# Optimization experiments

Hardware: AMD Instinct MI355X
Metric: run time of the kernel (lower is better)

The kernel has to match this reference:

```python
import jax, jax.numpy as jnp
import numpy as np

# GE2E batch structure: N_SPK speakers, M_UTT utterances each (grouped contiguously),
# first half enrollment (-> centroid), second half test.
N_SPK, M_UTT, D = 1024, 32, 512
M_ENR = M_UTT // 2
EPS = 1e-8  # F.cosine_similarity default eps (clamps norms)


def setup_inputs() -> dict:
    key = jax.random.key(0)
    emb = jax.random.normal(key, (N_SPK * M_UTT, D), dtype=jnp.float32)
    labels = jnp.repeat(jnp.arange(N_SPK, dtype=jnp.int64), M_UTT)
    alpha = jnp.asarray(10.0, dtype=jnp.float32)
    beta = jnp.asarray(-5.0, dtype=jnp.float32)
    return {"embeddings": emb, "labels": labels, "alpha": alpha, "beta": beta}


def reference(embeddings, labels, alpha, beta):
    # labels are contiguously grouped: label i occupies rows [i*M_UTT, (i+1)*M_UTT)
    emb = embeddings.reshape(N_SPK, M_UTT, D)
    enroll = emb[:, :M_ENR]          # [N, M_enr, D]
    test = emb[:, M_ENR:]            # [N, M_tst, D]
    centroid = enroll.mean(axis=1)   # [N, D]

    cent_n = centroid / jnp.maximum(
        jnp.linalg.norm(centroid, axis=-1, keepdims=True), EPS)
    test_n = test / jnp.maximum(
        jnp.linalg.norm(test, axis=-1, keepdims=True), EPS)

    # S[i, j, t] = alpha * cos(centroid_i, test_{j,t}) + beta
    S = alpha * jnp.einsum('id,jtd->ijt', cent_n, test_n) + beta
    E = jnp.exp(S)                                   # [N, N, M_tst]

    idx = jnp.arange(N_SPK)
    pos_sum = E[idx, idx].sum(axis=-1)               # diag: own test vs own centroid
    neg_sum = E.sum(axis=(1, 2)) - pos_sum           # all other speakers' test utts

    loss = (jnp.log(neg_sum) - jnp.log(pos_sum)).mean()
    return loss
```

## Files before the change

kernel.cpp:

```cpp
#include <hip/hip_runtime.h>
#include <math.h>

#define N_SPK 1024
#define M_UTT 32
#define M_ENR 16
#define M_TEST 16
#define D 512
#define N_TEST_ROWS (N_SPK * M_TEST)


typedef __attribute__((ext_vector_type(4))) float f32x4;
typedef __attribute__((ext_vector_type(8))) short short8;
typedef __attribute__((ext_vector_type(8))) unsigned short ushort8;

typedef const __attribute__((address_space(1))) void g_void;
typedef __attribute__((address_space(3))) void lds_void;

__device__ __forceinline__ unsigned short f2bf(float f) {
    unsigned int u = __float_as_uint(f);
    u += 0x7FFF + ((u >> 16) & 1);
    return (unsigned short)(u >> 16);
}

__global__ __launch_bounds__(256) void prep_kernel(const float* __restrict__ emb,
                                                   unsigned short* __restrict__ cent,
                                                   unsigned short* __restrict__ test,
                                                   float* __restrict__ g_row,
                                                   float* __restrict__ g_pos) {
    const int b = blockIdx.x;
    const int tid = threadIdx.x;
    const int lane = tid & 63;
    const int wid = tid >> 6;

    if (b < 4) {
        g_row[b * 256 + tid] = 0.f;
        g_pos[b * 256 + tid] = 0.f;
    }

    if (b < N_SPK) {
        const float* base = emb + (size_t)b * M_UTT * D;
        float a0 = 0.f, a1 = 0.f;
#pragma unroll
        for (int u = 0; u < M_ENR; ++u) {
            a0 += base[u * D + tid];
            a1 += base[u * D + tid + 256];
        }
        a0 *= (1.f / 16.f);
        a1 *= (1.f / 16.f);
        float ss = a0 * a0 + a1 * a1;
#pragma unroll
        for (int m = 1; m < 64; m <<= 1) ss += __shfl_xor(ss, m, 64);
        __shared__ float wss[4];
        if (lane == 0) wss[wid] = ss;
        __syncthreads();
        const float tot = wss[0] + wss[1] + wss[2] + wss[3];
        const float inv = 1.f / fmaxf(sqrtf(tot), 1e-8f);
        cent[b * D + tid] = f2bf(a0 * inv);
        cent[b * D + tid + 256] = f2bf(a1 * inv);
    } else {
        const int r = (b - N_SPK) * 4 + wid;
        const int s = r >> 4, t = r & 15;
        const float* row = emb + ((size_t)s * M_UTT + M_ENR + t) * D;
        const f32x4* rv = (const f32x4*)row;
        const f32x4 v0 = rv[lane * 2];
        const f32x4 v1 = rv[lane * 2 + 1];
        float ss = v0[0]*v0[0] + v0[1]*v0[1] + v0[2]*v0[2] + v0[3]*v0[3]
                 + v1[0]*v1[0] + v1[1]*v1[1] + v1[2]*v1[2] + v1[3]*v1[3];
#pragma unroll
        for (int m = 1; m < 64; m <<= 1) ss += __shfl_xor(ss, m, 64);
        const float inv = 1.f / fmaxf(sqrtf(ss), 1e-8f);
        ushort8 o;
        o[0] = f2bf(v0[0] * inv); o[1] = f2bf(v0[1] * inv);
        o[2] = f2bf(v0[2] * inv); o[3] = f2bf(v0[3] * inv);
        o[4] = f2bf(v1[0] * inv); o[5] = f2bf(v1[1] * inv);
        o[6] = f2bf(v1[2] * inv); o[7] = f2bf(v1[3] * inv);
        *(ushort8*)&test[(size_t)r * D + lane * 8] = o;
    }
}

__global__ __launch_bounds__(512, 2) void gemm_kernel(const unsigned short* __restrict__ A,
                                                      const unsigned short* __restrict__ B,
                                                      const float* __restrict__ alpha_p,
                                                      const float* __restrict__ beta_p,
                                                      float* __restrict__ g_row,
                                                      float* __restrict__ g_pos) {
    __shared__ __align__(16) unsigned short As[128 * 512];
    __shared__ float rowsum[128];
    __shared__ float possum[128];

    const int tid = threadIdx.x;
    const int lane = tid & 63;
    const int w = tid >> 6;

    const int raw = blockIdx.x;
    const int wg = (raw & 7) * 32 + (raw >> 3);
    const int bi = wg & 7;
    const int bj = wg >> 3;
    const int row0 = bi * 128, col0 = bj * 512;
    const bool has_diag = ((bj >> 2) == bi);

#pragma unroll
    for (int it = 0; it < 16; ++it) {
        const int r = it * 8 + w;
        const int src = (row0 + r) * D + ((lane * 8) ^ ((r & 7) << 3));
        __builtin_amdgcn_global_load_lds((g_void*)&A[src],
                                         (lds_void*)&As[r * D],
                                         16, 0, 0);
    }
    if (tid < 128) { rowsum[tid] = 0.f; possum[tid] = 0.f; }

    const float alpha = *alpha_p;
    const float beta = *beta_p;

    const int bcol = col0 + w * 64;
    const unsigned short* bp[4];
#pragma unroll
    for (int ni = 0; ni < 4; ++ni)
        bp[ni] = &B[(size_t)(bcol + ni * 16 + (lane & 15)) * D + (lane >> 4) * 8];

    const int hs = ((lane >> 4) * 8) ^ ((lane & 7) << 3);
    const int arow_base = (lane & 15) * D;

    f32x4 acc[8][4] = {};
    short8 bf0[4], bf1[4];

#define LOADB(dst, kk)                                             \
    {                                                              \
        const int kp_ = (kk);                                      \
        _Pragma("unroll") for (int ni = 0; ni < 4; ++ni)           \
            dst[ni] = *(const short8*)(bp[ni] + kp_);              \
    }

#define STEP(bfr, kk)                                                          \
    {                                                                          \
        const int ofs_ = (kk) ^ hs;                                            \
        _Pragma("unroll") for (int mi = 0; mi < 8; ++mi) {                     \
            const short8 af_ = *(const short8*)&As[mi * 16 * D + arow_base + ofs_]; \
            _Pragma("unroll") for (int ni = 0; ni < 4; ++ni)                   \
                acc[mi][ni] = __builtin_amdgcn_mfma_f32_16x16x32_bf16(         \
                    af_, bfr[ni], acc[mi][ni], 0, 0, 0);                       \
        }                                                                      \
    }

    LOADB(bf0, 0);
    __syncthreads();

    for (int ko = 0; ko < D; ko += 64) {
        LOADB(bf1, ko + 32);
        STEP(bf0, ko);
        LOADB(bf0, (ko + 64) & (D - 1));
        STEP(bf1, ko + 32);
    }

#pragma unroll
    for (int mi = 0; mi < 8; ++mi) {
#pragma unroll
        for (int r = 0; r < 4; ++r) {
            const int lrow = mi * 16 + ((lane >> 4) << 2) + r;
            const int grow = row0 + lrow;
            float tot = 0.f, pos = 0.f;
#pragma unroll
            for (int ni = 0; ni < 4; ++ni) {
                const int gcol = bcol + ni * 16 + (lane & 15);
                const float e = __expf(fmaf(alpha, acc[mi][ni][r], beta));
                tot += e;
                if (has_diag) pos += ((gcol >> 4) == grow) ? e : 0.f;
            }
#pragma unroll
            for (int m = 1; m < 16; m <<= 1) tot += __shfl_xor(tot, m, 64);
            if (has_diag) {
#pragma unroll
                for (int m = 1; m < 16; m <<= 1) pos += __shfl_xor(pos, m, 64);
            }
            if ((lane & 15) == 0) {
                atomicAdd(&rowsum[lrow], tot);
                if (has_diag) atomicAdd(&possum[lrow], pos);
            }
        }
    }
    __syncthreads();
    if (tid < 128) {
        atomicAdd(&g_row[row0 + tid], rowsum[tid]);
        if (has_diag) atomicAdd(&g_pos[row0 + tid], possum[tid]);
    }
#undef LOADB
#undef STEP
}

__global__ __launch_bounds__(1024) void finalize_kernel(const float* __restrict__ g_row,
                                                        const float* __restrict__ g_pos,
                                                        float* __restrict__ out) {
    __shared__ float red[1024];
    const int i = threadIdx.x;
    const float pos = g_pos[i];
    const float neg = g_row[i] - pos;
    red[i] = logf(fmaxf(neg, 1e-30f)) - logf(fmaxf(pos, 1e-30f));
    __syncthreads();
    for (int s = 512; s > 0; s >>= 1) {
        if (i < s) red[i] += red[i + s];
        __syncthreads();
    }
    if (i == 0) out[0] = red[0] * (1.f / 1024.f);
}

extern "C" void kernel_launch(void* const* d_in, const int* in_sizes, int n_in,
                              void* d_out, int out_size, void* d_ws, size_t ws_size,
                              hipStream_t stream) {
    const float* emb = (const float*)d_in[0];
    const float* alpha_p = (const float*)d_in[2];
    const float* beta_p = (const float*)d_in[3];

    unsigned short* cent = (unsigned short*)d_ws;
    unsigned short* test = cent + (size_t)N_SPK * D;
    float* g_row = (float*)(test + (size_t)N_TEST_ROWS * D);
    float* g_pos = g_row + N_SPK;

    prep_kernel<<<N_SPK + N_TEST_ROWS / 4, 256, 0, stream>>>(emb, cent, test, g_row, g_pos);

    gemm_kernel<<<256, 512, 0, stream>>>(cent, test, alpha_p, beta_p, g_row, g_pos);

    finalize_kernel<<<1, 1024, 0, stream>>>(g_row, g_pos, (float*)d_out);
}
```

Baseline: 49.09 us.

## Fuse finalize into GEMM via last-block counter and restructure epilogue reductions

Drops the separate finalize kernel. The last GEMM block to finish, found through an atomic counter that prep_kernel resets, now computes the log-ratio mean. The MFMA operands are swapped so each lane holds one centroid row, which turns the per-row 16-lane shuffle reductions into two cross-group shuffles and cuts the LDS atomics. Other changes: the B-fragment prefetch is double-buffered further ahead, the launch-bounds occupancy hint drops from 2 to 1, and centroid loads and stores are vectorised. The aim is to remove one kernel launch and reduce epilogue overhead. The cost is a serialized tail on the last block and possible register-pressure changes.

```diff
diff --git a/kernel.cpp b/kernel.cpp
--- a/kernel.cpp
+++ b/kernel.cpp
@@ -7,6 +7,7 @@
 #define M_TEST 16
 #define D 512
 #define N_TEST_ROWS (N_SPK * M_TEST)
+#define NBLK_GEMM 256
 
 
 typedef __attribute__((ext_vector_type(4))) float f32x4;
@@ -26,7 +27,8 @@
                                                    unsigned short* __restrict__ cent,
                                                    unsigned short* __restrict__ test,
                                                    float* __restrict__ g_row,
-                                                   float* __restrict__ g_pos) {
+                                                   float* __restrict__ g_pos,
+                                                   unsigned int* __restrict__ cnt) {
     const int b = blockIdx.x;
     const int tid = threadIdx.x;
     const int lane = tid & 63;
@@ -35,15 +37,16 @@
     if (b < 4) {
         g_row[b * 256 + tid] = 0.f;
         g_pos[b * 256 + tid] = 0.f;
+        if (b == 0 && tid == 0) *cnt = 0u;
     }
 
     if (b < N_SPK) {
-        const float* base = emb + (size_t)b * M_UTT * D;
+        const float2* base2 = (const float2*)(emb + (size_t)b * M_UTT * D);
         float a0 = 0.f, a1 = 0.f;
 #pragma unroll
         for (int u = 0; u < M_ENR; ++u) {
-            a0 += base[u * D + tid];
-            a1 += base[u * D + tid + 256];
+            const float2 v = base2[u * 256 + tid];
+            a0 += v.x; a1 += v.y;
         }
         a0 *= (1.f / 16.f);
         a1 *= (1.f / 16.f);
@@ -55,8 +58,10 @@
         __syncthreads();
         const float tot = wss[0] + wss[1] + wss[2] + wss[3];
         const float inv = 1.f / fmaxf(sqrtf(tot), 1e-8f);
-        cent[b * D + tid] = f2bf(a0 * inv);
-        cent[b * D + tid + 256] = f2bf(a1 * inv);
+        ushort2 o2;
+        o2.x = f2bf(a0 * inv);
+        o2.y = f2bf(a1 * inv);
+        *(ushort2*)&cent[b * D + 2 * tid] = o2;
     } else {
         const int r = (b - N_SPK) * 4 + wid;
         const int s = r >> 4, t = r & 15;
@@ -78,19 +83,24 @@
     }
 }
 
-__global__ __launch_bounds__(512, 2) void gemm_kernel(const unsigned short* __restrict__ A,
+__global__ __launch_bounds__(512, 1) void gemm_kernel(const unsigned short* __restrict__ A,
                                                       const unsigned short* __restrict__ B,
                                                       const float* __restrict__ alpha_p,
                                                       const float* __restrict__ beta_p,
                                                       float* __restrict__ g_row,
-                                                      float* __restrict__ g_pos) {
+                                                      float* __restrict__ g_pos,
+                                                      unsigned int* __restrict__ cnt,
+                                                      float* __restrict__ out) {
     __shared__ __align__(16) unsigned short As[128 * 512];
-    __shared__ float rowsum[128];
-    __shared__ float possum[128];
+    __shared__ float tsum[128];
+    __shared__ float psum[128];
+    __shared__ unsigned int last_flag;
+    __shared__ float ws2[8];
 
     const int tid = threadIdx.x;
     const int lane = tid & 63;
     const int w = tid >> 6;
+    const int l15 = lane & 15;
 
     const int raw = blockIdx.x;
     const int wg = (raw & 7) * 32 + (raw >> 3);
@@ -104,10 +114,9 @@
         const int r = it * 8 + w;
         const int src = (row0 + r) * D + ((lane * 8) ^ ((r & 7) << 3));
         __builtin_amdgcn_global_load_lds((g_void*)&A[src],
-                                         (lds_void*)&As[r * D],
-                                         16, 0, 0);
-    }
-    if (tid < 128) { rowsum[tid] = 0.f; possum[tid] = 0.f; }
+                                         (lds_void*)&As[r * D], 16, 0, 0);
+    }
+    if (tid < 128) { tsum[tid] = 0.f; psum[tid] = 0.f; }
 
     const float alpha = *alpha_p;
     const float beta = *beta_p;
@@ -116,19 +125,18 @@
     const unsigned short* bp[4];
 #pragma unroll
     for (int ni = 0; ni < 4; ++ni)
-        bp[ni] = &B[(size_t)(bcol + ni * 16 + (lane & 15)) * D + (lane >> 4) * 8];
+        bp[ni] = &B[(size_t)(bcol + ni * 16 + l15) * D + (lane >> 4) * 8];
 
     const int hs = ((lane >> 4) * 8) ^ ((lane & 7) << 3);
-    const int arow_base = (lane & 15) * D;
+    const int arow_base = l15 * D;
 
     f32x4 acc[8][4] = {};
-    short8 bf0[4], bf1[4];
-
-#define LOADB(dst, kk)                                             \
-    {                                                              \
-        const int kp_ = (kk);                                      \
-        _Pragma("unroll") for (int ni = 0; ni < 4; ++ni)           \
-            dst[ni] = *(const short8*)(bp[ni] + kp_);              \
+    short8 b0[4], b1[4];
+
+#define LOADB(dst, kk)                                              \
+    {                                                               \
+        _Pragma("unroll") for (int ni = 0; ni < 4; ++ni)            \
+            dst[ni] = *(const short8*)(bp[ni] + (kk));              \
     }
 
 #define STEP(bfr, kk)                                                          \
@@ -138,69 +146,73 @@
             const short8 af_ = *(const short8*)&As[mi * 16 * D + arow_base + ofs_]; \
             _Pragma("unroll") for (int ni = 0; ni < 4; ++ni)                   \
                 acc[mi][ni] = __builtin_amdgcn_mfma_f32_16x16x32_bf16(         \
-                    af_, bfr[ni], acc[mi][ni], 0, 0, 0);                       \
+                    bfr[ni], af_, acc[mi][ni], 0, 0, 0);                       \
         }                                                                      \
     }
 
-    LOADB(bf0, 0);
+    LOADB(b0, 0); LOADB(b1, 32);
     __syncthreads();
 
     for (int ko = 0; ko < D; ko += 64) {
-        LOADB(bf1, ko + 32);
-        STEP(bf0, ko);
-        LOADB(bf0, (ko + 64) & (D - 1));
-        STEP(bf1, ko + 32);
-    }
+        STEP(b0, ko);       LOADB(b0, (ko + 64) & (D - 1));
+        STEP(b1, ko + 32);  LOADB(b1, (ko + 96) & (D - 1));
+    }
+#undef LOADB
+#undef STEP
 
 #pragma unroll
     for (int mi = 0; mi < 8; ++mi) {
-#pragma unroll
-        for (int r = 0; r < 4; ++r) {
-            const int lrow = mi * 16 + ((lane >> 4) << 2) + r;
-            const int grow = row0 + lrow;
-            float tot = 0.f, pos = 0.f;
-#pragma unroll
-            for (int ni = 0; ni < 4; ++ni) {
-                const int gcol = bcol + ni * 16 + (lane & 15);
+        const int gs = row0 + mi * 16 + l15;
+        float t = 0.f, p = 0.f;
+#pragma unroll
+        for (int ni = 0; ni < 4; ++ni) {
+#pragma unroll
+            for (int r = 0; r < 4; ++r) {
                 const float e = __expf(fmaf(alpha, acc[mi][ni][r], beta));
-                tot += e;
-                if (has_diag) pos += ((gcol >> 4) == grow) ? e : 0.f;
+                t += e;
+                if (has_diag) {
+                    const int tc = bcol + ni * 16 + ((lane >> 4) << 2) + r;
+                    p += ((tc >> 4) == gs) ? e : 0.f;
+                }
             }
-#pragma unroll
-            for (int m = 1; m < 16; m <<= 1) tot += __shfl_xor(tot, m, 64);
-            if (has_diag) {
-#pragma unroll
-                for (int m = 1; m < 16; m <<= 1) pos += __shfl_xor(pos, m, 64);
-            }
-            if ((lane & 15) == 0) {
-                atomicAdd(&rowsum[lrow], tot);
-                if (has_diag) atomicAdd(&possum[lrow], pos);
-            }
+        }
+        t += __shfl_xor(t, 16, 64);
+        t += __shfl_xor(t, 32, 64);
+        if (lane < 16) atomicAdd(&tsum[mi * 16 + l15], t);
+        if (has_diag) {
+            p += __shfl_xor(p, 16, 64);
+            p += __shfl_xor(p, 32, 64);
+            if (lane < 16) atomicAdd(&psum[mi * 16 + l15], p);
         }
     }
     __syncthreads();
     if (tid < 128) {
-        atomicAdd(&g_row[row0 + tid], rowsum[tid]);
-        if (has_diag) atomicAdd(&g_pos[row0 + tid], possum[tid]);
-    }
-#undef LOADB
-#undef STEP
-}
-
-__global__ __launch_bounds__(1024) void finalize_kernel(const float* __restrict__ g_row,
-                                                        const float* __restrict__ g_pos,
-                                                        float* __restrict__ out) {
-    __shared__ float red[1024];
-    const int i = threadIdx.x;
-    const float pos = g_pos[i];
-    const float neg = g_row[i] - pos;
-    red[i] = logf(fmaxf(neg, 1e-30f)) - logf(fmaxf(pos, 1e-30f));
+        atomicAdd(&g_row[row0 + tid], tsum[tid]);
+        if (has_diag) atomicAdd(&g_pos[row0 + tid], psum[tid]);
+    }
+
+    __threadfence();
+    if (tid == 0) last_flag = (atomicAdd(cnt, 1u) == (NBLK_GEMM - 1)) ? 1u : 0u;
     __syncthreads();
-    for (int s = 512; s > 0; s >>= 1) {
-        if (i < s) red[i] += red[i + s];
+    if (last_flag) {
+        __threadfence();
+        float v = 0.f;
+        for (int i = tid; i < N_SPK; i += 512) {
+            const float pos = g_pos[i];
+            const float neg = g_row[i] - pos;
+            v += logf(fmaxf(neg, 1e-30f)) - logf(fmaxf(pos, 1e-30f));
+        }
+#pragma unroll
+        for (int m = 1; m < 64; m <<= 1) v += __shfl_xor(v, m, 64);
+        if (lane == 0) ws2[w] = v;
         __syncthreads();
-    }
-    if (i == 0) out[0] = red[0] * (1.f / 1024.f);
+        if (tid == 0) {
+            float s = 0.f;
+#pragma unroll
+            for (int j = 0; j < 8; ++j) s += ws2[j];
+            out[0] = s * (1.f / 1024.f);
+        }
+    }
 }
 
 extern "C" void kernel_launch(void* const* d_in, const int* in_sizes, int n_in,
@@ -214,10 +226,11 @@
     unsigned short* test = cent + (size_t)N_SPK * D;
     float* g_row = (float*)(test + (size_t)N_TEST_ROWS * D);
     float* g_pos = g_row + N_SPK;
-
-    prep_kernel<<<N_SPK + N_TEST_ROWS / 4, 256, 0, stream>>>(emb, cent, test, g_row, g_pos);
-
-    gemm_kernel<<<256, 512, 0, stream>>>(cent, test, alpha_p, beta_p, g_row, g_pos);
-
-    finalize_kernel<<<1, 1024, 0, stream>>>(g_row, g_pos, (float*)d_out);
-}
+    unsigned int* cnt = (unsigned int*)(g_pos + N_SPK);
+
+    prep_kernel<<<N_SPK + N_TEST_ROWS / 4, 256, 0, stream>>>(emb, cent, test,
+                                                             g_row, g_pos, cnt);
+
+    gemm_kernel<<<NBLK_GEMM, 512, 0, stream>>>(cent, test, alpha_p, beta_p,
+                                               g_row, g_pos, cnt, (float*)d_out);
+}
```

New measurement: 71.36 us. 1.45x slower.
